# Kernel optimization log

Hardware: AMD Instinct MI355X
Metric: run time of the kernel (lower is better)

Reference implementation:

```python
import jax, jax.numpy as jnp
import numpy as np

NQ = 4  # qubits
NL = 2  # layers actually used by the circuit body
BATCH = 1048576

def _c64(a):
    return a.astype(jnp.complex64)

def _ry(t):
    # RY(t) = [[cos(t/2), -sin(t/2)], [sin(t/2), cos(t/2)]]; t scalar or [B]
    c, s = jnp.cos(t / 2), jnp.sin(t / 2)
    return _c64(jnp.stack([jnp.stack([c, -s], -1), jnp.stack([s, c], -1)], -2))

def _rx(t):
    # RX(t) = [[cos(t/2), -i sin(t/2)], [-i sin(t/2), cos(t/2)]]
    c, s = _c64(jnp.cos(t / 2)), _c64(jnp.sin(t / 2))
    return jnp.stack([jnp.stack([c, -1j * s], -1), jnp.stack([-1j * s, c], -1)], -2)

def _rz(t):
    # RZ(t) = diag(exp(-i t/2), exp(i t/2))
    ph = _c64(t / 2)
    em, ep = jnp.exp(-1j * ph), jnp.exp(1j * ph)
    z = jnp.zeros_like(em)
    return jnp.stack([jnp.stack([em, z], -1), jnp.stack([z, ep], -1)], -2)

def _apply1q(state, gate, wire):
    # state: [B, 2,2,2,2]; gate: [2,2] (shared) or [B,2,2] (per-sample angle)
    s = jnp.moveaxis(state, wire + 1, -1)
    if gate.ndim == 3:
        out = jnp.einsum('b...j,bij->b...i', s, gate)
    else:
        out = jnp.einsum('b...j,ij->b...i', s, gate)
    return jnp.moveaxis(out, -1, wire + 1)

def _cnot(state, c, t):
    # bring control to axis 1, target to axis 2; flip target where control==1
    s = jnp.moveaxis(state, (c + 1, t + 1), (1, 2))
    s = jnp.stack([s[:, 0], jnp.flip(s[:, 1], axis=1)], axis=1)
    return jnp.moveaxis(s, (1, 2), (c + 1, t + 1))

def _circuit(x, weights):
    B = x.shape[0]
    state = jnp.zeros((B, 2 ** NQ), jnp.complex64).at[:, 0].set(1.0)
    state = state.reshape((B,) + (2,) * NQ)
    # angle encoding: RY(x_i) on wire i (per-sample angles)
    for i in range(NQ):
        state = _apply1q(state, _ry(x[:, i]), i)
    w = weights.reshape(NL, NQ, 3)
    for layer in range(NL):
        for i in range(NQ):
            state = _apply1q(state, _rx(w[layer, i, 0]), i)
            state = _apply1q(state, _ry(w[layer, i, 1]), i)
            state = _apply1q(state, _rz(w[layer, i, 2]), i)
        for i in range(NQ - 1):
            state = _cnot(state, i, i + 1)
        state = _cnot(state, NQ - 1, 0)
    # expval PauliZ on wire 0: +|amp|^2 for q0=0, -|amp|^2 for q0=1
    p = state.real ** 2 + state.imag ** 2
    p = p.reshape(B, 2, -1).sum(-1)
    return (p[:, 0] - p[:, 1]).astype(jnp.float32)

def setup_inputs() -> dict:
    key = jax.random.key(0)
    k1, k2 = jax.random.split(key)
    x = jax.random.normal(k1, (BATCH, NQ), jnp.float32)
    weights = jax.random.normal(k2, (NL * NQ * 3,), jnp.float32)
    return {"x": x, "weights": weights}

def reference(x, weights):
    return _circuit(x, weights)
```

## Files before the change

kernel.cpp:

```cpp
#include <hip/hip_runtime.h>
#include <hip/hip_bf16.h>


#define VEC 4

__global__ void build_K_kernel(const float* __restrict__ w, float* __restrict__ K) {
    __shared__ float Ur[16][17], Ui[16][17];
    __shared__ float Msh[256];

    const int t = threadIdx.x;
    const int j = t >> 4;
    const int k = t & 15;

    float ur = (k == j) ? 1.0f : 0.0f;
    float ui = 0.0f;

    #pragma unroll
    for (int layer = 0; layer < 2; ++layer) {
        #pragma unroll
        for (int q = 0; q < 4; ++q) {
            const int bit = 3 - q;
            const int str = 1 << bit;
            const int kb = (k >> bit) & 1;
            float c, s, pr, pi, nr, ni;
            __sincosf(w[(layer * 4 + q) * 3 + 0] * 0.5f, &s, &c);
            pr = __shfl_xor(ur, str);
            pi = __shfl_xor(ui, str);
            nr = c * ur + s * pi;
            ni = c * ui - s * pr;
            ur = nr; ui = ni;
            __sincosf(w[(layer * 4 + q) * 3 + 1] * 0.5f, &s, &c);
            pr = __shfl_xor(ur, str);
            pi = __shfl_xor(ui, str);
            {
                const float sg = kb ? s : -s;
                nr = c * ur + sg * pr;
                ni = c * ui + sg * pi;
            }
            ur = nr; ui = ni;
            __sincosf(w[(layer * 4 + q) * 3 + 2] * 0.5f, &s, &c);
            {
                const float sz = kb ? s : -s;
                nr = c * ur - sz * ui;
                ni = c * ui + sz * ur;
            }
            ur = nr; ui = ni;
        }
        #pragma unroll
        for (int g = 0; g < 4; ++g) {
            const int cw = g;
            const int tw = (g + 1) & 3;
            const int bc = 3 - cw, bt = 3 - tw;
            const float pr = __shfl_xor(ur, 1 << bt);
            const float pi = __shfl_xor(ui, 1 << bt);
            const bool ctl = (k >> bc) & 1;
            ur = ctl ? pr : ur;
            ui = ctl ? pi : ui;
        }
    }

    Ur[k][j] = ur;
    Ui[k][j] = ui;
    __syncthreads();

    {
        const int a = t >> 4, b = t & 15;
        float acc = 0.0f;
        #pragma unroll
        for (int kk = 0; kk < 16; ++kk) {
            const float v2 = Ur[kk][a] * Ur[kk][b] + Ui[kk][a] * Ui[kk][b];
            acc += (kk & 8) ? -v2 : v2;
        }
        Msh[t] = acc;
    }
    __syncthreads();

    if (t < 81) {
        const int d0 = t / 27, d1 = (t / 9) % 3, d2 = (t / 3) % 3, d3 = t % 3;
        const int gd[4] = {d3, d2, d1, d0};
        float sum = 0.0f;
        #pragma unroll
        for (int m = 0; m < 16; ++m) {
            int a2 = 0, b2 = 0;
            float sign = 1.0f;
            #pragma unroll
            for (int p = 0; p < 4; ++p) {
                const int cp = (m >> p) & 1;
                if (gd[p] == 2) { a2 |= cp << p; b2 |= (1 - cp) << p; }
                else {
                    a2 |= cp << p; b2 |= cp << p;
                    if (gd[p] == 1 && cp) sign = -sign;
                }
            }
            sum += sign * Msh[a2 * 16 + b2];
        }
        K[t] = sum * 0.0625f;
    }
}

__global__ __launch_bounds__(256) void qnn_eval_kernel(
    const float4* __restrict__ x, const float* __restrict__ K,
    float* __restrict__ out, int n) {
    __shared__ float Ks[81];
    if (threadIdx.x < 81) Ks[threadIdx.x] = K[threadIdx.x];
    __syncthreads();

    const int gid = blockIdx.x * blockDim.x + threadIdx.x;
    const int stride = gridDim.x * blockDim.x;

    for (int i0 = gid; i0 < n; i0 += stride * VEC) {
        int idx[VEC];
        bool ok[VEC];
        float C[VEC][4], S[VEC][4];
        #pragma unroll
        for (int v = 0; v < VEC; ++v) {
            const int ii = i0 + v * stride;
            ok[v] = ii < n;
            idx[v] = ok[v] ? ii : (n - 1);
            const float4 xv = x[idx[v]];
            __sincosf(xv.x, &S[v][0], &C[v][0]);
            __sincosf(xv.y, &S[v][1], &C[v][1]);
            __sincosf(xv.z, &S[v][2], &C[v][2]);
            __sincosf(xv.w, &S[v][3], &C[v][3]);
        }

        float r[VEC];
        #pragma unroll
        for (int d0 = 0; d0 < 3; ++d0) {
            float a1[VEC];
            #pragma unroll
            for (int d1 = 0; d1 < 3; ++d1) {
                float a2[VEC];
                #pragma unroll
                for (int d2 = 0; d2 < 3; ++d2) {
                    const int base = ((d0 * 3 + d1) * 3 + d2) * 3;
                    const float k0 = Ks[base], k1 = Ks[base + 1], k2 = Ks[base + 2];
                    #pragma unroll
                    for (int v = 0; v < VEC; ++v) {
                        const float tt = fmaf(k2, S[v][3], fmaf(k1, C[v][3], k0));
                        if (d2 == 0) a2[v] = tt;
                        else a2[v] = fmaf(tt, (d2 == 1) ? C[v][2] : S[v][2], a2[v]);
                    }
                }
                #pragma unroll
                for (int v = 0; v < VEC; ++v) {
                    if (d1 == 0) a1[v] = a2[v];
                    else a1[v] = fmaf(a2[v], (d1 == 1) ? C[v][1] : S[v][1], a1[v]);
                }
            }
            #pragma unroll
            for (int v = 0; v < VEC; ++v) {
                if (d0 == 0) r[v] = a1[v];
                else r[v] = fmaf(a1[v], (d0 == 1) ? C[v][0] : S[v][0], r[v]);
            }
        }

        #pragma unroll
        for (int v = 0; v < VEC; ++v)
            if (ok[v]) out[idx[v]] = r[v];
    }
}

extern "C" void kernel_launch(void* const* d_in, const int* in_sizes, int n_in,
                              void* d_out, int out_size, void* d_ws, size_t ws_size,
                              hipStream_t stream) {
    const float* x = (const float*)d_in[0];
    const float* w = (const float*)d_in[1];
    float* out = (float*)d_out;
    float* K = (float*)d_ws;

    const int n = in_sizes[0] / 4;

    build_K_kernel<<<1, 256, 0, stream>>>(w, K);

    const int block = 256;
    const int per_block = block * VEC;
    int grid = (n + per_block - 1) / per_block;
    if (grid < 1) grid = 1;
    qnn_eval_kernel<<<grid, block, 0, stream>>>((const float4*)x, K, out, n);
}
```

Measured before the change: 69.49 us.

## Fuse K-build into eval kernel and use packed f32x2 FMAs

Merges the single-block coefficient-building kernel into the evaluation kernel, so each block recomputes the 81-entry K tensor in shared memory. This removes a separate launch and the workspace round trip. The polynomial evaluation now runs on two-wide float vectors so the compiler can emit packed FMA instructions, with VEC doubled to 8 and the grid capped at 2048 blocks. The trade-off is that every block repeats the small K computation (shuffles, sincos, a 16x16 reduction), which adds per-block latency before the eval loop starts.

```diff
diff --git a/kernel.cpp b/kernel.cpp
--- a/kernel.cpp
+++ b/kernel.cpp
@@ -2,65 +2,74 @@
 #include <hip/hip_bf16.h>
 
 
-#define VEC 4
-
-__global__ void build_K_kernel(const float* __restrict__ w, float* __restrict__ K) {
+typedef float f32x2 __attribute__((ext_vector_type(2)));
+
+#define BLOCK 256
+#define NPAIR 4
+#define VEC (2 * NPAIR)
+
+__global__ __launch_bounds__(BLOCK, 4) void qnn_fused_kernel(
+    const float4* __restrict__ x, const float* __restrict__ w,
+    float* __restrict__ out, int n) {
+
     __shared__ float Ur[16][17], Ui[16][17];
     __shared__ float Msh[256];
+    __shared__ float Ks[81];
 
     const int t = threadIdx.x;
-    const int j = t >> 4;
-    const int k = t & 15;
-
-    float ur = (k == j) ? 1.0f : 0.0f;
-    float ui = 0.0f;
-
-    #pragma unroll
-    for (int layer = 0; layer < 2; ++layer) {
-        #pragma unroll
-        for (int q = 0; q < 4; ++q) {
-            const int bit = 3 - q;
-            const int str = 1 << bit;
-            const int kb = (k >> bit) & 1;
-            float c, s, pr, pi, nr, ni;
-            __sincosf(w[(layer * 4 + q) * 3 + 0] * 0.5f, &s, &c);
-            pr = __shfl_xor(ur, str);
-            pi = __shfl_xor(ui, str);
-            nr = c * ur + s * pi;
-            ni = c * ui - s * pr;
-            ur = nr; ui = ni;
-            __sincosf(w[(layer * 4 + q) * 3 + 1] * 0.5f, &s, &c);
-            pr = __shfl_xor(ur, str);
-            pi = __shfl_xor(ui, str);
-            {
-                const float sg = kb ? s : -s;
-                nr = c * ur + sg * pr;
-                ni = c * ui + sg * pi;
-            }
-            ur = nr; ui = ni;
-            __sincosf(w[(layer * 4 + q) * 3 + 2] * 0.5f, &s, &c);
-            {
-                const float sz = kb ? s : -s;
-                nr = c * ur - sz * ui;
-                ni = c * ui + sz * ur;
-            }
-            ur = nr; ui = ni;
-        }
-        #pragma unroll
-        for (int g = 0; g < 4; ++g) {
-            const int cw = g;
-            const int tw = (g + 1) & 3;
-            const int bc = 3 - cw, bt = 3 - tw;
-            const float pr = __shfl_xor(ur, 1 << bt);
-            const float pi = __shfl_xor(ui, 1 << bt);
-            const bool ctl = (k >> bc) & 1;
-            ur = ctl ? pr : ur;
-            ui = ctl ? pi : ui;
-        }
-    }
-
-    Ur[k][j] = ur;
-    Ui[k][j] = ui;
+
+    {
+        const int j = t >> 4;
+        const int k = t & 15;
+        float ur = (k == j) ? 1.0f : 0.0f;
+        float ui = 0.0f;
+
+        #pragma unroll
+        for (int layer = 0; layer < 2; ++layer) {
+            #pragma unroll
+            for (int q = 0; q < 4; ++q) {
+                const int bit = 3 - q;
+                const int str = 1 << bit;
+                const int kb = (k >> bit) & 1;
+                float c, s, pr, pi, nr, ni;
+                __sincosf(w[(layer * 4 + q) * 3 + 0] * 0.5f, &s, &c);
+                pr = __shfl_xor(ur, str);
+                pi = __shfl_xor(ui, str);
+                nr = c * ur + s * pi;
+                ni = c * ui - s * pr;
+                ur = nr; ui = ni;
+                __sincosf(w[(layer * 4 + q) * 3 + 1] * 0.5f, &s, &c);
+                pr = __shfl_xor(ur, str);
+                pi = __shfl_xor(ui, str);
+                {
+                    const float sg = kb ? s : -s;
+                    nr = c * ur + sg * pr;
+                    ni = c * ui + sg * pi;
+                }
+                ur = nr; ui = ni;
+                __sincosf(w[(layer * 4 + q) * 3 + 2] * 0.5f, &s, &c);
+                {
+                    const float sz = kb ? s : -s;
+                    nr = c * ur - sz * ui;
+                    ni = c * ui + sz * ur;
+                }
+                ur = nr; ui = ni;
+            }
+            #pragma unroll
+            for (int g = 0; g < 4; ++g) {
+                const int cw = g;
+                const int tw = (g + 1) & 3;
+                const int bc = 3 - cw, bt = 3 - tw;
+                const float pr = __shfl_xor(ur, 1 << bt);
+                const float pi = __shfl_xor(ui, 1 << bt);
+                const bool ctl = (k >> bc) & 1;
+                ur = ctl ? pr : ur;
+                ui = ctl ? pi : ui;
+            }
+        }
+        Ur[k][j] = ur;
+        Ui[k][j] = ui;
+    }
     __syncthreads();
 
     {
@@ -94,70 +103,86 @@
             }
             sum += sign * Msh[a2 * 16 + b2];
         }
-        K[t] = sum * 0.0625f;
-    }
-}
-
-__global__ __launch_bounds__(256) void qnn_eval_kernel(
-    const float4* __restrict__ x, const float* __restrict__ K,
-    float* __restrict__ out, int n) {
-    __shared__ float Ks[81];
-    if (threadIdx.x < 81) Ks[threadIdx.x] = K[threadIdx.x];
+        Ks[t] = sum * 0.0625f;
+    }
     __syncthreads();
 
-    const int gid = blockIdx.x * blockDim.x + threadIdx.x;
-    const int stride = gridDim.x * blockDim.x;
+    const int gid = blockIdx.x * BLOCK + t;
+    const int stride = gridDim.x * BLOCK;
 
     for (int i0 = gid; i0 < n; i0 += stride * VEC) {
-        int idx[VEC];
-        bool ok[VEC];
-        float C[VEC][4], S[VEC][4];
-        #pragma unroll
-        for (int v = 0; v < VEC; ++v) {
-            const int ii = i0 + v * stride;
-            ok[v] = ii < n;
-            idx[v] = ok[v] ? ii : (n - 1);
-            const float4 xv = x[idx[v]];
-            __sincosf(xv.x, &S[v][0], &C[v][0]);
-            __sincosf(xv.y, &S[v][1], &C[v][1]);
-            __sincosf(xv.z, &S[v][2], &C[v][2]);
-            __sincosf(xv.w, &S[v][3], &C[v][3]);
-        }
-
-        float r[VEC];
+        int idxA[NPAIR], idxB[NPAIR];
+        bool okA[NPAIR], okB[NPAIR];
+        f32x2 C2[NPAIR][4], S2[NPAIR][4];
+
+        #pragma unroll
+        for (int u = 0; u < NPAIR; ++u) {
+            {
+                const int ii = i0 + (2 * u) * stride;
+                okA[u] = ii < n;
+                idxA[u] = okA[u] ? ii : (n - 1);
+                const float4 xv = x[idxA[u]];
+                float s, c;
+                __sincosf(xv.x, &s, &c); C2[u][0].x = c; S2[u][0].x = s;
+                __sincosf(xv.y, &s, &c); C2[u][1].x = c; S2[u][1].x = s;
+                __sincosf(xv.z, &s, &c); C2[u][2].x = c; S2[u][2].x = s;
+                __sincosf(xv.w, &s, &c); C2[u][3].x = c; S2[u][3].x = s;
+            }
+            {
+                const int ii = i0 + (2 * u + 1) * stride;
+                okB[u] = ii < n;
+                idxB[u] = okB[u] ? ii : (n - 1);
+                const float4 xv = x[idxB[u]];
+                float s, c;
+                __sincosf(xv.x, &s, &c); C2[u][0].y = c; S2[u][0].y = s;
+                __sincosf(xv.y, &s, &c); C2[u][1].y = c; S2[u][1].y = s;
+                __sincosf(xv.z, &s, &c); C2[u][2].y = c; S2[u][2].y = s;
+                __sincosf(xv.w, &s, &c); C2[u][3].y = c; S2[u][3].y = s;
+            }
+        }
+
+        f32x2 r[NPAIR];
         #pragma unroll
         for (int d0 = 0; d0 < 3; ++d0) {
-            float a1[VEC];
+            f32x2 a1[NPAIR];
             #pragma unroll
             for (int d1 = 0; d1 < 3; ++d1) {
-                float a2[VEC];
+                f32x2 a2[NPAIR];
                 #pragma unroll
                 for (int d2 = 0; d2 < 3; ++d2) {
                     const int base = ((d0 * 3 + d1) * 3 + d2) * 3;
                     const float k0 = Ks[base], k1 = Ks[base + 1], k2 = Ks[base + 2];
+                    const f32x2 k0v = {k0, k0}, k1v = {k1, k1}, k2v = {k2, k2};
                     #pragma unroll
-                    for (int v = 0; v < VEC; ++v) {
-                        const float tt = fmaf(k2, S[v][3], fmaf(k1, C[v][3], k0));
-                        if (d2 == 0) a2[v] = tt;
-                        else a2[v] = fmaf(tt, (d2 == 1) ? C[v][2] : S[v][2], a2[v]);
+                    for (int u = 0; u < NPAIR; ++u) {
+                        const f32x2 tt = __builtin_elementwise_fma(
+                            k2v, S2[u][3],
+                            __builtin_elementwise_fma(k1v, C2[u][3], k0v));
+                        if (d2 == 0) a2[u] = tt;
+                        else a2[u] = __builtin_elementwise_fma(
+                                 tt, (d2 == 1) ? C2[u][2] : S2[u][2], a2[u]);
                     }
                 }
                 #pragma unroll
-                for (int v = 0; v < VEC; ++v) {
-                    if (d1 == 0) a1[v] = a2[v];
-                    else a1[v] = fmaf(a2[v], (d1 == 1) ? C[v][1] : S[v][1], a1[v]);
-                }
-            }
-            #pragma unroll
-            for (int v = 0; v < VEC; ++v) {
-                if (d0 == 0) r[v] = a1[v];
-                else r[v] = fmaf(a1[v], (d0 == 1) ? C[v][0] : S[v][0], r[v]);
-            }
-        }
-
-        #pragma unroll
-        for (int v = 0; v < VEC; ++v)
-            if (ok[v]) out[idx[v]] = r[v];
+                for (int u = 0; u < NPAIR; ++u) {
+                    if (d1 == 0) a1[u] = a2[u];
+                    else a1[u] = __builtin_elementwise_fma(
+                             a2[u], (d1 == 1) ? C2[u][1] : S2[u][1], a1[u]);
+                }
+            }
+            #pragma unroll
+            for (int u = 0; u < NPAIR; ++u) {
+                if (d0 == 0) r[u] = a1[u];
+                else r[u] = __builtin_elementwise_fma(
+                         a1[u], (d0 == 1) ? C2[u][0] : S2[u][0], r[u]);
+            }
+        }
+
+        #pragma unroll
+        for (int u = 0; u < NPAIR; ++u) {
+            if (okA[u]) out[idxA[u]] = r[u].x;
+            if (okB[u]) out[idxB[u]] = r[u].y;
+        }
     }
 }
 
@@ -167,15 +192,12 @@
     const float* x = (const float*)d_in[0];
     const float* w = (const float*)d_in[1];
     float* out = (float*)d_out;
-    float* K = (float*)d_ws;
 
     const int n = in_sizes[0] / 4;
 
-    build_K_kernel<<<1, 256, 0, stream>>>(w, K);
-
-    const int block = 256;
-    const int per_block = block * VEC;
-    int grid = (n + per_block - 1) / per_block;
+    int grid = (n + BLOCK * VEC - 1) / (BLOCK * VEC);
     if (grid < 1) grid = 1;
-    qnn_eval_kernel<<<grid, block, 0, stream>>>((const float4*)x, K, out, n);
+    if (grid > 2048) grid = 2048;
+
+    qnn_fused_kernel<<<grid, BLOCK, 0, stream>>>((const float4*)x, w, out, n);
 }
```

Result: slower. 117.3 us (+68.8%).

## Fuse K-matrix construction into eval kernel and keep coefficients in scalar registers

Applied to the files above, without the earlier changes.

Merges the single-block build_K kernel into the batch evaluation kernel, so every block recomputes the 81 Pauli-basis coefficients redundantly in shared memory. This removes a second kernel launch and the global round trip for K. The coefficients are then broadcast into uniform registers via readfirstlane instead of being read from LDS inside the loop. Per-sample evaluation is also reorganised to process one vector element at a time to reduce register pressure. The grid is capped at 4096 blocks and launch bounds request 4 blocks per CU. The cost is redundant per-block setup work (sincos, shuffles, a 16x16 reduction) and extra barriers before the streaming loop.

```diff
diff --git a/kernel.cpp b/kernel.cpp
--- a/kernel.cpp
+++ b/kernel.cpp
@@ -2,65 +2,71 @@
 #include <hip/hip_bf16.h>
 
 
+#define BLOCK 256
 #define VEC 4
 
-__global__ void build_K_kernel(const float* __restrict__ w, float* __restrict__ K) {
+__global__ __launch_bounds__(BLOCK, 4) void qnn_fused_kernel(
+    const float4* __restrict__ x, const float* __restrict__ w,
+    float* __restrict__ out, int n) {
+
     __shared__ float Ur[16][17], Ui[16][17];
     __shared__ float Msh[256];
+    __shared__ float Ks[81];
 
     const int t = threadIdx.x;
-    const int j = t >> 4;
-    const int k = t & 15;
 
-    float ur = (k == j) ? 1.0f : 0.0f;
-    float ui = 0.0f;
+    {
+        const int j = t >> 4;
+        const int k = t & 15;
+        float ur = (k == j) ? 1.0f : 0.0f;
+        float ui = 0.0f;
 
-    #pragma unroll
-    for (int layer = 0; layer < 2; ++layer) {
         #pragma unroll
-        for (int q = 0; q < 4; ++q) {
-            const int bit = 3 - q;
-            const int str = 1 << bit;
-            const int kb = (k >> bit) & 1;
-            float c, s, pr, pi, nr, ni;
-            __sincosf(w[(layer * 4 + q) * 3 + 0] * 0.5f, &s, &c);
-            pr = __shfl_xor(ur, str);
-            pi = __shfl_xor(ui, str);
-            nr = c * ur + s * pi;
-            ni = c * ui - s * pr;
-            ur = nr; ui = ni;
-            __sincosf(w[(layer * 4 + q) * 3 + 1] * 0.5f, &s, &c);
-            pr = __shfl_xor(ur, str);
-            pi = __shfl_xor(ui, str);
-            {
-                const float sg = kb ? s : -s;
-                nr = c * ur + sg * pr;
-                ni = c * ui + sg * pi;
+        for (int layer = 0; layer < 2; ++layer) {
+            #pragma unroll
+            for (int q = 0; q < 4; ++q) {
+                const int bit = 3 - q;
+                const int str = 1 << bit;
+                const int kb = (k >> bit) & 1;
+                float c, s, pr, pi, nr, ni;
+                __sincosf(w[(layer * 4 + q) * 3 + 0] * 0.5f, &s, &c);
+                pr = __shfl_xor(ur, str);
+                pi = __shfl_xor(ui, str);
+                nr = c * ur + s * pi;
+                ni = c * ui - s * pr;
+                ur = nr; ui = ni;
+                __sincosf(w[(layer * 4 + q) * 3 + 1] * 0.5f, &s, &c);
+                pr = __shfl_xor(ur, str);
+                pi = __shfl_xor(ui, str);
+                {
+                    const float sg = kb ? s : -s;
+                    nr = c * ur + sg * pr;
+                    ni = c * ui + sg * pi;
+                }
+                ur = nr; ui = ni;
+                __sincosf(w[(layer * 4 + q) * 3 + 2] * 0.5f, &s, &c);
+                {
+                    const float sz = kb ? s : -s;
+                    nr = c * ur - sz * ui;
+                    ni = c * ui + sz * ur;
+                }
+                ur = nr; ui = ni;
             }
-            ur = nr; ui = ni;
-            __sincosf(w[(layer * 4 + q) * 3 + 2] * 0.5f, &s, &c);
-            {
-                const float sz = kb ? s : -s;
-                nr = c * ur - sz * ui;
-                ni = c * ui + sz * ur;
+            #pragma unroll
+            for (int g = 0; g < 4; ++g) {
+                const int cw = g;
+                const int tw = (g + 1) & 3;
+                const int bc = 3 - cw, bt = 3 - tw;
+                const float pr = __shfl_xor(ur, 1 << bt);
+                const float pi = __shfl_xor(ui, 1 << bt);
+                const bool ctl = (k >> bc) & 1;
+                ur = ctl ? pr : ur;
+                ui = ctl ? pi : ui;
             }
-            ur = nr; ui = ni;
         }
-        #pragma unroll
-        for (int g = 0; g < 4; ++g) {
-            const int cw = g;
-            const int tw = (g + 1) & 3;
-            const int bc = 3 - cw, bt = 3 - tw;
-            const float pr = __shfl_xor(ur, 1 << bt);
-            const float pi = __shfl_xor(ui, 1 << bt);
-            const bool ctl = (k >> bc) & 1;
-            ur = ctl ? pr : ur;
-            ui = ctl ? pi : ui;
-        }
+        Ur[k][j] = ur;
+        Ui[k][j] = ui;
     }
-
-    Ur[k][j] = ur;
-    Ui[k][j] = ui;
     __syncthreads();
 
     {
@@ -94,70 +100,62 @@
             }
             sum += sign * Msh[a2 * 16 + b2];
         }
-        K[t] = sum * 0.0625f;
+        Ks[t] = sum * 0.0625f;
     }
-}
-
-__global__ __launch_bounds__(256) void qnn_eval_kernel(
-    const float4* __restrict__ x, const float* __restrict__ K,
-    float* __restrict__ out, int n) {
-    __shared__ float Ks[81];
-    if (threadIdx.x < 81) Ks[threadIdx.x] = K[threadIdx.x];
     __syncthreads();
 
-    const int gid = blockIdx.x * blockDim.x + threadIdx.x;
-    const int stride = gridDim.x * blockDim.x;
+    float kk[81];
+    #pragma unroll
+    for (int i = 0; i < 81; ++i)
+        kk[i] = __uint_as_float(
+            (unsigned)__builtin_amdgcn_readfirstlane(__float_as_uint(Ks[i])));
+
+    const int gid = blockIdx.x * BLOCK + t;
+    const int stride = gridDim.x * BLOCK;
 
     for (int i0 = gid; i0 < n; i0 += stride * VEC) {
         int idx[VEC];
         bool ok[VEC];
-        float C[VEC][4], S[VEC][4];
+        float4 xv[VEC];
         #pragma unroll
         for (int v = 0; v < VEC; ++v) {
             const int ii = i0 + v * stride;
             ok[v] = ii < n;
             idx[v] = ok[v] ? ii : (n - 1);
-            const float4 xv = x[idx[v]];
-            __sincosf(xv.x, &S[v][0], &C[v][0]);
-            __sincosf(xv.y, &S[v][1], &C[v][1]);
-            __sincosf(xv.z, &S[v][2], &C[v][2]);
-            __sincosf(xv.w, &S[v][3], &C[v][3]);
-        }
-
-        float r[VEC];
-        #pragma unroll
-        for (int d0 = 0; d0 < 3; ++d0) {
-            float a1[VEC];
-            #pragma unroll
-            for (int d1 = 0; d1 < 3; ++d1) {
-                float a2[VEC];
-                #pragma unroll
-                for (int d2 = 0; d2 < 3; ++d2) {
-                    const int base = ((d0 * 3 + d1) * 3 + d2) * 3;
-                    const float k0 = Ks[base], k1 = Ks[base + 1], k2 = Ks[base + 2];
-                    #pragma unroll
-                    for (int v = 0; v < VEC; ++v) {
-                        const float tt = fmaf(k2, S[v][3], fmaf(k1, C[v][3], k0));
-                        if (d2 == 0) a2[v] = tt;
-                        else a2[v] = fmaf(tt, (d2 == 1) ? C[v][2] : S[v][2], a2[v]);
-                    }
-                }
-                #pragma unroll
-                for (int v = 0; v < VEC; ++v) {
-                    if (d1 == 0) a1[v] = a2[v];
-                    else a1[v] = fmaf(a2[v], (d1 == 1) ? C[v][1] : S[v][1], a1[v]);
-                }
-            }
-            #pragma unroll
-            for (int v = 0; v < VEC; ++v) {
-                if (d0 == 0) r[v] = a1[v];
-                else r[v] = fmaf(a1[v], (d0 == 1) ? C[v][0] : S[v][0], r[v]);
-            }
+            xv[v] = x[idx[v]];
         }
 
         #pragma unroll
-        for (int v = 0; v < VEC; ++v)
-            if (ok[v]) out[idx[v]] = r[v];
+        for (int v = 0; v < VEC; ++v) {
+            float C[4], S[4];
+            __sincosf(xv[v].x, &S[0], &C[0]);
+            __sincosf(xv[v].y, &S[1], &C[1]);
+            __sincosf(xv[v].z, &S[2], &C[2]);
+            __sincosf(xv[v].w, &S[3], &C[3]);
+
+            float r = 0.0f;
+            #pragma unroll
+            for (int d0 = 0; d0 < 3; ++d0) {
+                float a1 = 0.0f;
+                #pragma unroll
+                for (int d1 = 0; d1 < 3; ++d1) {
+                    float a2 = 0.0f;
+                    #pragma unroll
+                    for (int d2 = 0; d2 < 3; ++d2) {
+                        const int base = ((d0 * 3 + d1) * 3 + d2) * 3;
+                        const float tt = fmaf(kk[base + 2], S[3],
+                                         fmaf(kk[base + 1], C[3], kk[base]));
+                        if (d2 == 0) a2 = tt;
+                        else a2 = fmaf(tt, (d2 == 1) ? C[2] : S[2], a2);
+                    }
+                    if (d1 == 0) a1 = a2;
+                    else a1 = fmaf(a2, (d1 == 1) ? C[1] : S[1], a1);
+                }
+                if (d0 == 0) r = a1;
+                else r = fmaf(a1, (d0 == 1) ? C[0] : S[0], r);
+            }
+            if (ok[v]) out[idx[v]] = r;
+        }
     }
 }
 
@@ -167,15 +165,12 @@
     const float* x = (const float*)d_in[0];
     const float* w = (const float*)d_in[1];
     float* out = (float*)d_out;
-    float* K = (float*)d_ws;
 
     const int n = in_sizes[0] / 4;
 
-    build_K_kernel<<<1, 256, 0, stream>>>(w, K);
+    int grid = (n + BLOCK * VEC - 1) / (BLOCK * VEC);
+    if (grid < 1) grid = 1;
+    if (grid > 4096) grid = 4096;
 
-    const int block = 256;
-    const int per_block = block * VEC;
-    int grid = (n + per_block - 1) / per_block;
-    if (grid < 1) grid = 1;
-    qnn_eval_kernel<<<grid, block, 0, stream>>>((const float4*)x, K, out, n);
+    qnn_fused_kernel<<<grid, BLOCK, 0, stream>>>((const float4*)x, w, out, n);
 }
```

Result: no change. 70.39 us (+1.3%).

## Fuse coefficient build into eval kernel, recomputing K per block

Applied to the files above, without the earlier changes.

Merges the single-block kernel that builds the 81 coefficients with the per-sample evaluation kernel, so each block recomputes the coefficients in shared memory. This removes a second launch and the serialized dependency on a one-block kernel. In exchange every block repeats the unitary construction (sincos, shuffles, reductions) before it starts its main work. It also issues all four float4 loads before the sincos calls so the loads can overlap.

```diff
diff --git a/kernel.cpp b/kernel.cpp
--- a/kernel.cpp
+++ b/kernel.cpp
@@ -2,65 +2,71 @@
 #include <hip/hip_bf16.h>
 
 
+#define BLOCK 256
 #define VEC 4
 
-__global__ void build_K_kernel(const float* __restrict__ w, float* __restrict__ K) {
+__global__ __launch_bounds__(BLOCK) void qnn_fused_kernel(
+    const float4* __restrict__ x, const float* __restrict__ w,
+    float* __restrict__ out, int n) {
+
     __shared__ float Ur[16][17], Ui[16][17];
     __shared__ float Msh[256];
+    __shared__ float Ks[81];
 
     const int t = threadIdx.x;
-    const int j = t >> 4;
-    const int k = t & 15;
 
-    float ur = (k == j) ? 1.0f : 0.0f;
-    float ui = 0.0f;
+    {
+        const int j = t >> 4;
+        const int k = t & 15;
+        float ur = (k == j) ? 1.0f : 0.0f;
+        float ui = 0.0f;
 
-    #pragma unroll
-    for (int layer = 0; layer < 2; ++layer) {
         #pragma unroll
-        for (int q = 0; q < 4; ++q) {
-            const int bit = 3 - q;
-            const int str = 1 << bit;
-            const int kb = (k >> bit) & 1;
-            float c, s, pr, pi, nr, ni;
-            __sincosf(w[(layer * 4 + q) * 3 + 0] * 0.5f, &s, &c);
-            pr = __shfl_xor(ur, str);
-            pi = __shfl_xor(ui, str);
-            nr = c * ur + s * pi;
-            ni = c * ui - s * pr;
-            ur = nr; ui = ni;
-            __sincosf(w[(layer * 4 + q) * 3 + 1] * 0.5f, &s, &c);
-            pr = __shfl_xor(ur, str);
-            pi = __shfl_xor(ui, str);
-            {
-                const float sg = kb ? s : -s;
-                nr = c * ur + sg * pr;
-                ni = c * ui + sg * pi;
+        for (int layer = 0; layer < 2; ++layer) {
+            #pragma unroll
+            for (int q = 0; q < 4; ++q) {
+                const int bit = 3 - q;
+                const int str = 1 << bit;
+                const int kb = (k >> bit) & 1;
+                float c, s, pr, pi, nr, ni;
+                __sincosf(w[(layer * 4 + q) * 3 + 0] * 0.5f, &s, &c);
+                pr = __shfl_xor(ur, str);
+                pi = __shfl_xor(ui, str);
+                nr = c * ur + s * pi;
+                ni = c * ui - s * pr;
+                ur = nr; ui = ni;
+                __sincosf(w[(layer * 4 + q) * 3 + 1] * 0.5f, &s, &c);
+                pr = __shfl_xor(ur, str);
+                pi = __shfl_xor(ui, str);
+                {
+                    const float sg = kb ? s : -s;
+                    nr = c * ur + sg * pr;
+                    ni = c * ui + sg * pi;
+                }
+                ur = nr; ui = ni;
+                __sincosf(w[(layer * 4 + q) * 3 + 2] * 0.5f, &s, &c);
+                {
+                    const float sz = kb ? s : -s;
+                    nr = c * ur - sz * ui;
+                    ni = c * ui + sz * ur;
+                }
+                ur = nr; ui = ni;
             }
-            ur = nr; ui = ni;
-            __sincosf(w[(layer * 4 + q) * 3 + 2] * 0.5f, &s, &c);
-            {
-                const float sz = kb ? s : -s;
-                nr = c * ur - sz * ui;
-                ni = c * ui + sz * ur;
+            #pragma unroll
+            for (int g = 0; g < 4; ++g) {
+                const int cw = g;
+                const int tw = (g + 1) & 3;
+                const int bc = 3 - cw, bt = 3 - tw;
+                const float pr = __shfl_xor(ur, 1 << bt);
+                const float pi = __shfl_xor(ui, 1 << bt);
+                const bool ctl = (k >> bc) & 1;
+                ur = ctl ? pr : ur;
+                ui = ctl ? pi : ui;
             }
-            ur = nr; ui = ni;
         }
-        #pragma unroll
-        for (int g = 0; g < 4; ++g) {
-            const int cw = g;
-            const int tw = (g + 1) & 3;
-            const int bc = 3 - cw, bt = 3 - tw;
-            const float pr = __shfl_xor(ur, 1 << bt);
-            const float pi = __shfl_xor(ui, 1 << bt);
-            const bool ctl = (k >> bc) & 1;
-            ur = ctl ? pr : ur;
-            ui = ctl ? pi : ui;
-        }
+        Ur[k][j] = ur;
+        Ui[k][j] = ui;
     }
-
-    Ur[k][j] = ur;
-    Ui[k][j] = ui;
     __syncthreads();
 
     {
@@ -94,34 +100,32 @@
             }
             sum += sign * Msh[a2 * 16 + b2];
         }
-        K[t] = sum * 0.0625f;
+        Ks[t] = sum * 0.0625f;
     }
-}
-
-__global__ __launch_bounds__(256) void qnn_eval_kernel(
-    const float4* __restrict__ x, const float* __restrict__ K,
-    float* __restrict__ out, int n) {
-    __shared__ float Ks[81];
-    if (threadIdx.x < 81) Ks[threadIdx.x] = K[threadIdx.x];
     __syncthreads();
 
-    const int gid = blockIdx.x * blockDim.x + threadIdx.x;
-    const int stride = gridDim.x * blockDim.x;
+    const int gid = blockIdx.x * BLOCK + t;
+    const int stride = gridDim.x * BLOCK;
 
     for (int i0 = gid; i0 < n; i0 += stride * VEC) {
         int idx[VEC];
         bool ok[VEC];
-        float C[VEC][4], S[VEC][4];
+        float4 xv[VEC];
         #pragma unroll
         for (int v = 0; v < VEC; ++v) {
             const int ii = i0 + v * stride;
             ok[v] = ii < n;
             idx[v] = ok[v] ? ii : (n - 1);
-            const float4 xv = x[idx[v]];
-            __sincosf(xv.x, &S[v][0], &C[v][0]);
-            __sincosf(xv.y, &S[v][1], &C[v][1]);
-            __sincosf(xv.z, &S[v][2], &C[v][2]);
-            __sincosf(xv.w, &S[v][3], &C[v][3]);
+            xv[v] = x[idx[v]];
+        }
+
+        float C[VEC][4], S[VEC][4];
+        #pragma unroll
+        for (int v = 0; v < VEC; ++v) {
+            __sincosf(xv[v].x, &S[v][0], &C[v][0]);
+            __sincosf(xv[v].y, &S[v][1], &C[v][1]);
+            __sincosf(xv[v].z, &S[v][2], &C[v][2]);
+            __sincosf(xv[v].w, &S[v][3], &C[v][3]);
         }
 
         float r[VEC];
@@ -167,15 +171,12 @@
     const float* x = (const float*)d_in[0];
     const float* w = (const float*)d_in[1];
     float* out = (float*)d_out;
-    float* K = (float*)d_ws;
 
     const int n = in_sizes[0] / 4;
 
-    build_K_kernel<<<1, 256, 0, stream>>>(w, K);
+    int grid = (n + BLOCK * VEC - 1) / (BLOCK * VEC);
+    if (grid < 1) grid = 1;
+    if (grid > 4096) grid = 4096;
 
-    const int block = 256;
-    const int per_block = block * VEC;
-    int grid = (n + per_block - 1) / per_block;
-    if (grid < 1) grid = 1;
-    qnn_eval_kernel<<<grid, block, 0, stream>>>((const float4*)x, K, out, n);
+    qnn_fused_kernel<<<grid, BLOCK, 0, stream>>>((const float4*)x, w, out, n);
 }
```

Result: no change. 69.87 us (+0.6%).
